# Performance work log

Measured on AMD Instinct MI355X. Metric: run time of the kernel, lower is better.

Reference implementation:

```python
import jax, jax.numpy as jnp
import numpy as np
from jax import lax

PATCH = 9
DILATION = 1
EPS = 1e-6


def _l2norm(x):
    # L2-normalize over channel dim (dim=1), eps added to sum of squares before sqrt
    norm = jnp.sqrt(jnp.sum(x * x, axis=1, keepdims=True) + EPS)
    return x / norm


def setup_inputs() -> dict:
    key = jax.random.key(0)
    k1, k2 = jax.random.split(key)
    feature1 = jax.random.normal(k1, (4, 64, 64, 64), dtype=jnp.float32)
    feature2 = jax.random.normal(k2, (4, 64, 64, 64), dtype=jnp.float32)
    return {"feature1": feature1, "feature2": feature2}


def _correlation(f1, f2, patch, dilation):
    # SpatialCorrelationSampler with ks=1, stride=1, pad=0:
    # corr[b, pi, pj, y, x] = sum_c f1[b,c,y,x] * f2[b,c,y+dy,x+dx]
    # dy = (pi - patch//2)*dilation, dx = (pj - patch//2)*dilation; OOB = 0.
    b, c, h, w = f1.shape
    half = (patch // 2) * dilation
    f2p = jnp.pad(f2, ((0, 0), (0, 0), (half, half), (half, half)))
    d = jnp.arange(patch, dtype=jnp.int32) * dilation  # offsets into padded map
    offs = jnp.stack(jnp.meshgrid(d, d, indexing="ij"), axis=-1).reshape(-1, 2)  # [P^2, 2]

    def one_disp(off):
        f2s = lax.dynamic_slice(f2p, (0, 0, off[0], off[1]), (b, c, h, w))
        return jnp.sum(f1 * f2s, axis=1)  # [b, h, w]

    corr = lax.map(one_disp, offs)  # [P^2, b, h, w] (sequential -> low peak memory)
    return jnp.transpose(corr, (1, 0, 2, 3))  # [b, P^2, h, w]


def reference(feature1, feature2):
    f1 = _l2norm(feature1)
    f2 = _l2norm(feature2)
    b, c, h, w = f1.shape
    corr = _correlation(f1, f2, PATCH, DILATION)  # [b, P^2, h, w]
    corr = corr.reshape(b, PATCH * PATCH, h * w)
    return jax.nn.relu(corr)
```

## Files before the change

kernel.cpp:

```cpp
#include <hip/hip_runtime.h>

#define BB 4
#define CC 64
#define HH 64
#define WW 64
#define PATCH 9
#define HALF 4
#define P2 81
#define HW (HH * WW)

__global__ __launch_bounds__(128) void norm_kernel(const float* __restrict__ f1,
                                                   const float* __restrict__ f2,
                                                   float* __restrict__ invn) {
    int p = blockIdx.x * 128 + threadIdx.x;
    int feat = p >> 14;
    int idx = p & 16383;
    const float* base = (feat ? f2 : f1) + (idx >> 12) * (CC * HW) + (idx & 4095);
    float s = 0.f;
#pragma unroll
    for (int c = 0; c < CC; ++c) {
        float v = base[c * HW];
        s += v * v;
    }
    invn[p] = rsqrtf(s + 1e-6f);
}

__global__ __launch_bounds__(192) void corr_kernel(const float* __restrict__ f1,
                                                   const float* __restrict__ f2,
                                                   const float* __restrict__ invn,
                                                   float* __restrict__ out) {
    __shared__ float ldsB[CC * 72];

    const int tid = threadIdx.x;
    const int bid = blockIdx.x;
    const int dy = bid % PATCH;
    const int y  = (bid / PATCH) & 63;
    const int b  = bid / (PATCH * HH);
    const int x  = tid & 63;
    const int g  = tid >> 6;
    const int gy2 = y + dy - HALF;

    float* ob = out + b * P2 * HW + y * WW + x;

    if ((unsigned)gy2 >= HH) {
#pragma unroll
        for (int j = 0; j < 3; ++j)
            ob[(dy * PATCH + g * 3 + j) * HW] = 0.f;
        return;
    }

    const float* f1r = f1 + b * CC * HW + y * WW;
    const float* f2r = f2 + b * CC * HW + gy2 * WW;

    for (int i = tid; i < CC * 16; i += 192) {
        int c = i >> 4, k = i & 15;
        float4 v = *(const float4*)(f2r + c * HW + k * 4);
        *(float4*)(&ldsB[c * 72 + 4 + k * 4]) = v;
    }
    for (int j = tid; j < CC * 8; j += 192) {
        int c = j >> 3, e = j & 7;
        ldsB[c * 72 + (e < 4 ? e : e + 64)] = 0.f;
    }
    __syncthreads();

    float acc0 = 0.f, acc1 = 0.f, acc2 = 0.f;
    const int boff = x + g * 3;
#pragma unroll
    for (int c0 = 0; c0 < CC; c0 += 16) {
        float a[16];
#pragma unroll
        for (int j = 0; j < 16; ++j) a[j] = f1r[(c0 + j) * HW + x];
#pragma unroll
        for (int j = 0; j < 16; ++j) {
            const float* br = &ldsB[(c0 + j) * 72 + boff];
            acc0 = fmaf(a[j], br[0], acc0);
            acc1 = fmaf(a[j], br[1], acc1);
            acc2 = fmaf(a[j], br[2], acc2);
        }
    }

    const float s1 = invn[b * HW + y * WW + x];
    const float* in2 = invn + BB * HW + b * HW + gy2 * WW;
    float accs[3] = {acc0, acc1, acc2};
#pragma unroll
    for (int j = 0; j < 3; ++j) {
        int dx = g * 3 + j;
        int xx = x + dx - HALF;
        xx = min(max(xx, 0), WW - 1);
        float s2 = in2[xx];
        ob[(dy * PATCH + dx) * HW] = fmaxf(accs[j] * s1 * s2, 0.f);
    }
}

extern "C" void kernel_launch(void* const* d_in, const int* in_sizes, int n_in,
                              void* d_out, int out_size, void* d_ws, size_t ws_size,
                              hipStream_t stream) {
    const float* f1 = (const float*)d_in[0];
    const float* f2 = (const float*)d_in[1];
    float* out = (float*)d_out;
    float* invn = (float*)d_ws;

    norm_kernel<<<256, 128, 0, stream>>>(f1, f2, invn);
    corr_kernel<<<BB * HH * PATCH, 192, 0, stream>>>(f1, f2, invn, out);
}
```

Measured before the change: 72.75 us.

## Fuse L2 norm computation into correlation kernel and use packed float2 FMAs

Removes the separate norm kernel launch. Each block now computes the inverse norms of f2 from the LDS tile (padded zeros give eps) and the f1 norm from the values it already loads. The inner product loop is rewritten with 2-wide vector types so the compiler can emit packed FMA instructions. The norm work is recomputed redundantly in every block, which trades one extra launch and a global round trip for extra arithmetic and an added barrier.

```diff
diff --git a/kernel.cpp b/kernel.cpp
--- a/kernel.cpp
+++ b/kernel.cpp
@@ -9,27 +9,13 @@
 #define P2 81
 #define HW (HH * WW)
 
-__global__ __launch_bounds__(128) void norm_kernel(const float* __restrict__ f1,
-                                                   const float* __restrict__ f2,
-                                                   float* __restrict__ invn) {
-    int p = blockIdx.x * 128 + threadIdx.x;
-    int feat = p >> 14;
-    int idx = p & 16383;
-    const float* base = (feat ? f2 : f1) + (idx >> 12) * (CC * HW) + (idx & 4095);
-    float s = 0.f;
-#pragma unroll
-    for (int c = 0; c < CC; ++c) {
-        float v = base[c * HW];
-        s += v * v;
-    }
-    invn[p] = rsqrtf(s + 1e-6f);
-}
+typedef float v2f __attribute__((ext_vector_type(2)));
 
 __global__ __launch_bounds__(192) void corr_kernel(const float* __restrict__ f1,
                                                    const float* __restrict__ f2,
-                                                   const float* __restrict__ invn,
                                                    float* __restrict__ out) {
     __shared__ float ldsB[CC * 72];
+    __shared__ float ldsS[72];
 
     const int tid = threadIdx.x;
     const int bid = blockIdx.x;
@@ -63,7 +49,18 @@
     }
     __syncthreads();
 
-    float acc0 = 0.f, acc1 = 0.f, acc2 = 0.f;
+    if (tid < 72) {
+        v2f ss = {0.f, 0.f};
+#pragma unroll
+        for (int c = 0; c < CC; c += 2) {
+            v2f v = {ldsB[c * 72 + tid], ldsB[(c + 1) * 72 + tid]};
+            ss += v * v;
+        }
+        ldsS[tid] = rsqrtf(ss.x + ss.y + 1e-6f);
+    }
+
+    v2f acc0 = {0.f, 0.f}, acc1 = {0.f, 0.f}, acc2 = {0.f, 0.f};
+    v2f sacc = {0.f, 0.f};
     const int boff = x + g * 3;
 #pragma unroll
     for (int c0 = 0; c0 < CC; c0 += 16) {
@@ -71,23 +68,26 @@
 #pragma unroll
         for (int j = 0; j < 16; ++j) a[j] = f1r[(c0 + j) * HW + x];
 #pragma unroll
-        for (int j = 0; j < 16; ++j) {
+        for (int j = 0; j < 16; j += 2) {
+            v2f a2 = {a[j], a[j + 1]};
             const float* br = &ldsB[(c0 + j) * 72 + boff];
-            acc0 = fmaf(a[j], br[0], acc0);
-            acc1 = fmaf(a[j], br[1], acc1);
-            acc2 = fmaf(a[j], br[2], acc2);
+            v2f b0 = {br[0], br[72]};
+            v2f b1 = {br[1], br[73]};
+            v2f b2 = {br[2], br[74]};
+            acc0 += a2 * b0;
+            acc1 += a2 * b1;
+            acc2 += a2 * b2;
+            sacc += a2 * a2;
         }
     }
+    __syncthreads();
 
-    const float s1 = invn[b * HW + y * WW + x];
-    const float* in2 = invn + BB * HW + b * HW + gy2 * WW;
-    float accs[3] = {acc0, acc1, acc2};
+    const float s1 = rsqrtf(sacc.x + sacc.y + 1e-6f);
+    float accs[3] = {acc0.x + acc0.y, acc1.x + acc1.y, acc2.x + acc2.y};
 #pragma unroll
     for (int j = 0; j < 3; ++j) {
         int dx = g * 3 + j;
-        int xx = x + dx - HALF;
-        xx = min(max(xx, 0), WW - 1);
-        float s2 = in2[xx];
+        float s2 = ldsS[boff + j];
         ob[(dy * PATCH + dx) * HW] = fmaxf(accs[j] * s1 * s2, 0.f);
     }
 }
@@ -98,8 +98,7 @@
     const float* f1 = (const float*)d_in[0];
     const float* f2 = (const float*)d_in[1];
     float* out = (float*)d_out;
-    float* invn = (float*)d_ws;
+    (void)d_ws; (void)ws_size;
 
-    norm_kernel<<<256, 128, 0, stream>>>(f1, f2, invn);
-    corr_kernel<<<BB * HH * PATCH, 192, 0, stream>>>(f1, f2, invn, out);
+    corr_kernel<<<BB * HH * PATCH, 192, 0, stream>>>(f1, f2, out);
 }
```

New measurement: 70.72 us. 1.03x faster.
